# Kernel optimization log

Hardware: AMD Instinct MI355X
Metric: run time of the kernel (lower is better)

## Reference

```python
import jax, jax.numpy as jnp
import numpy as np

# Quantum kernel closed form:
#   Encoder applies RY(x_k) on wire k from |0>, then RY(-y_k); RY(-y)RY(x) = RY(x-y).
#   Amplitude of |0...0> = prod_k <0|RY(x_k - y_k)|0> = prod_k cos((x_k - y_k)/2).
#   kernel(x, y) = | prod_k cos((x_k - y_k)/2) |.
# Using cos(a-b) = cos a cos b + sin a sin b avoids forming explicit pairwise diffs twice.

def setup_inputs() -> dict:
    key = jax.random.key(0)
    x = jax.random.normal(key, (32, 1024, 4), dtype=jnp.float32)  # [B, S, n_wires]
    return {"x": x}


def reference(x) -> jnp.ndarray:
    c = jnp.cos(0.5 * x)  # [B, S, W]
    s = jnp.sin(0.5 * x)
    # cos((x_i,k - x_j,k)/2) for all pairs -> [B, S, S, W]
    term = c[:, :, None, :] * c[:, None, :, :] + s[:, :, None, :] * s[:, None, :, :]
    kernel_mat = jnp.abs(jnp.prod(term, axis=-1))  # [B, S, S]
    attn = jax.nn.softmax(kernel_mat, axis=-1)
    return jnp.matmul(attn, x)  # [B, S, W]
```

## Files before the change

kernel.cpp:

```cpp
#include <hip/hip_runtime.h>


typedef _Float16 f16x8 __attribute__((ext_vector_type(8)));
typedef _Float16 h2    __attribute__((ext_vector_type(2)));
typedef float    f32x16 __attribute__((ext_vector_type(16)));
typedef unsigned int u32x4 __attribute__((ext_vector_type(4)));

#define SQ 1024
#define NTHREADS 512
#define ROWS 64

#if __has_builtin(__builtin_amdgcn_permlane32_swap)
__device__ __forceinline__ void pl32swap(unsigned &a, unsigned &b) {
    auto r = __builtin_amdgcn_permlane32_swap(a, b, false, false);
    a = r[0]; b = r[1];
}
#else
__device__ __forceinline__ void pl32swap(unsigned &a, unsigned &b) {
    asm("v_permlane32_swap_b32 %0, %1" : "+v"(a), "+v"(b));
}
#endif

__device__ __forceinline__ unsigned pexp_abs(float a, float b) {
    auto tp = __builtin_amdgcn_cvt_pkrtz(fabsf(a), fabsf(b));
    h2 t = __builtin_bit_cast(h2, tp);
    const h2 C4 = {(_Float16)0.0695580f, (_Float16)0.0695580f};
    const h2 C3 = {(_Float16)0.1399810f, (_Float16)0.1399810f};
    const h2 C2 = {(_Float16)0.5100530f, (_Float16)0.5100530f};
    const h2 C1 = {(_Float16)0.9986730f, (_Float16)0.9986730f};
    const h2 C0 = {(_Float16)0.9999940f, (_Float16)0.9999940f};
    h2 p = __builtin_elementwise_fma(C4, t, C3);
    p = __builtin_elementwise_fma(p, t, C2);
    p = __builtin_elementwise_fma(p, t, C1);
    p = __builtin_elementwise_fma(p, t, C0);
    return __builtin_bit_cast(unsigned, p);
}

__global__ __launch_bounds__(NTHREADS, 4)
void qka_kernel(const float* __restrict__ x, float* __restrict__ out) {
    __shared__ f16x8 lds_F0[SQ];
    __shared__ f16x8 lds_F1[SQ];
    __shared__ f16x8 lds_XT[5 * 129];

    const int bid   = blockIdx.x;
    const int b     = bid >> 4;
    const int Ibase = (bid & 15) * ROWS;
    const int tid   = threadIdx.x;

    const float4* xb  = (const float4*)(x + (size_t)b * SQ * 4);
    _Float16*     xtp = (_Float16*)lds_XT;

    #pragma unroll
    for (int k = 0; k < SQ / NTHREADS; ++k) {
        int j = tid + k * NTHREADS;
        float4 v = xb[j];
        float c0 = __cosf(0.5f * v.x), s0 = __sinf(0.5f * v.x);
        float c1 = __cosf(0.5f * v.y), s1 = __sinf(0.5f * v.y);
        float c2 = __cosf(0.5f * v.z), s2 = __sinf(0.5f * v.z);
        float c3 = __cosf(0.5f * v.w), s3 = __sinf(0.5f * v.w);
        float m0 = c0 * c1, m1 = s0 * c1, m2 = c0 * s1, m3 = s0 * s1;
        float n0 = m0 * c2, n1 = m1 * c2, n2 = m2 * c2, n3 = m3 * c2;
        float n4 = m0 * s2, n5 = m1 * s2, n6 = m2 * s2, n7 = m3 * s2;
        f16x8 p0, p1;
        p0[0] = (_Float16)(n0 * c3); p0[1] = (_Float16)(n1 * c3);
        p0[2] = (_Float16)(n2 * c3); p0[3] = (_Float16)(n3 * c3);
        p0[4] = (_Float16)(n4 * c3); p0[5] = (_Float16)(n5 * c3);
        p0[6] = (_Float16)(n6 * c3); p0[7] = (_Float16)(n7 * c3);
        p1[0] = (_Float16)(n0 * s3); p1[1] = (_Float16)(n1 * s3);
        p1[2] = (_Float16)(n2 * s3); p1[3] = (_Float16)(n3 * s3);
        p1[4] = (_Float16)(n4 * s3); p1[5] = (_Float16)(n5 * s3);
        p1[6] = (_Float16)(n6 * s3); p1[7] = (_Float16)(n7 * s3);
        int sj = j ^ ((j >> 3) & 7);
        lds_F0[sj] = p0;
        lds_F1[sj] = p1;
        xtp[0 * 1032 + j] = (_Float16)v.x;
        xtp[1 * 1032 + j] = (_Float16)v.y;
        xtp[2 * 1032 + j] = (_Float16)v.z;
        xtp[3 * 1032 + j] = (_Float16)v.w;
        xtp[4 * 1032 + j] = (_Float16)1.0f;
    }
    __syncthreads();

    const int wid  = tid >> 6;
    const int q    = wid & 3;
    const int rt   = wid >> 2;
    const int lane = tid & 63;
    const int h    = lane >> 5;
    const int ln   = lane & 31;

    const f16x8* Fh = h ? lds_F1 : lds_F0;
    int ib = Ibase + rt * 32 + ln; ib ^= (ib >> 3) & 7;
    const f16x8 bfrag = Fh[ib];

    const int rowsel = (ln < 4) ? ln : 4;
    const int xbase  = rowsel * 129 + q * 32 + h;

    f32x16 oacc0 = (f32x16)(0.0f);
    f32x16 oacc1 = (f32x16)(0.0f);

    int ja0 = q * 256 + ln;
    f16x8 af0 = Fh[ja0 ^ ((ja0 >> 3) & 7)];
    f32x16 d = __builtin_amdgcn_mfma_f32_32x32x16_f16(
        af0, bfrag, (f32x16)(0.0f), 0, 0, 0);

    #pragma unroll 2
    for (int t = 0; t < 8; ++t) {
        f16x8 afn;
        if (t < 7) {
            int jn = q * 256 + (t + 1) * 32 + ln;
            afn = Fh[jn ^ ((jn >> 3) & 7)];
        }
        f16x8 xf0 = lds_XT[xbase + t * 4];
        f16x8 xf1 = lds_XT[xbase + t * 4 + 2];
        unsigned q0 = pexp_abs(d[0],  d[1]);
        unsigned q1 = pexp_abs(d[2],  d[3]);
        unsigned q2 = pexp_abs(d[4],  d[5]);
        unsigned q3 = pexp_abs(d[6],  d[7]);
        unsigned q4 = pexp_abs(d[8],  d[9]);
        unsigned q5 = pexp_abs(d[10], d[11]);
        unsigned q6 = pexp_abs(d[12], d[13]);
        unsigned q7 = pexp_abs(d[14], d[15]);
        f32x16 dn;
        if (t < 7)
            dn = __builtin_amdgcn_mfma_f32_32x32x16_f16(
                afn, bfrag, (f32x16)(0.0f), 0, 0, 0);
        pl32swap(q0, q2); pl32swap(q1, q3);
        pl32swap(q4, q6); pl32swap(q5, q7);
        u32x4 w0 = {q0, q1, q2, q3};
        u32x4 w1 = {q4, q5, q6, q7};
        f16x8 ef0 = __builtin_bit_cast(f16x8, w0);
        f16x8 ef1 = __builtin_bit_cast(f16x8, w1);
        oacc0 = __builtin_amdgcn_mfma_f32_32x32x16_f16(ef0, xf0, oacc0, 0, 0, 0);
        oacc1 = __builtin_amdgcn_mfma_f32_32x32x16_f16(ef1, xf1, oacc1, 0, 0, 0);
        if (t < 7) d = dn;
    }

    __syncthreads();
    float* ps = (float*)lds_F0;
    if (ln < 5) {
        #pragma unroll
        for (int r = 0; r < 16; ++r) {
            int m = (r & 3) + 8 * (r >> 2) + 4 * h;
            ps[(q * 64 + rt * 32 + m) * 8 + ln] = oacc0[r] + oacc1[r];
        }
    }
    __syncthreads();

    if (tid < ROWS) {
        float nx = 0.f, ny = 0.f, nz = 0.f, nw = 0.f, den = 0.f;
        #pragma unroll
        for (int qq = 0; qq < 4; ++qq) {
            const float* p = &ps[(qq * 64 + tid) * 8];
            nx += p[0]; ny += p[1]; nz += p[2]; nw += p[3]; den += p[4];
        }
        float inv = 1.0f / den;
        ((float4*)out)[(size_t)b * SQ + Ibase + tid] =
            make_float4(nx * inv, ny * inv, nz * inv, nw * inv);
    }
}

extern "C" void kernel_launch(void* const* d_in, const int* in_sizes, int n_in,
                              void* d_out, int out_size, void* d_ws, size_t ws_size,
                              hipStream_t stream) {
    const float* x = (const float*)d_in[0];
    float* out = (float*)d_out;
    dim3 grid(32 * (SQ / ROWS));
    dim3 block(NTHREADS);
    qka_kernel<<<grid, block, 0, stream>>>(x, out);
}
```

Baseline: 12.13 us.

## Precompute feature maps in a staging kernel and DMA them into LDS

Moves the per-token cos/sin feature-map computation and the x transpose into a separate staging kernel that writes fp16 features to workspace, once per batch instead of once per each of 16 row blocks. The main kernel then fills LDS with direct global-to-LDS loads, applying the swizzle on the global address side. This removes redundant transcendental work across blocks but adds a second launch and a round trip of the features through global memory.

Measured after the change: 17.70 us. 45.9% more time.

```diff
diff --git a/kernel.cpp b/kernel.cpp
--- a/kernel.cpp
+++ b/kernel.cpp
@@ -9,6 +9,13 @@
 #define SQ 1024
 #define NTHREADS 512
 #define ROWS 64
+#define XT_SLOTS 645
+#define XT_PITCH 1032
+
+#define F0_OFF 0
+#define F1_OFF (32 * 1024 * 16)
+#define XT_OFF (2 * 32 * 1024 * 16)
+#define XT_BATCH_BYTES (704 * 16)
 
 #if __has_builtin(__builtin_amdgcn_permlane32_swap)
 __device__ __forceinline__ void pl32swap(unsigned &a, unsigned &b) {
@@ -36,49 +43,73 @@
     return __builtin_bit_cast(unsigned, p);
 }
 
+__global__ __launch_bounds__(512)
+void qka_stage(const float* __restrict__ x, char* __restrict__ ws) {
+    const int bid = blockIdx.x;
+    const int b   = bid >> 1;
+    const int j   = ((bid & 1) << 9) + threadIdx.x;
+    float4 v = ((const float4*)(x + (size_t)b * SQ * 4))[j];
+    float c0 = __cosf(0.5f * v.x), s0 = __sinf(0.5f * v.x);
+    float c1 = __cosf(0.5f * v.y), s1 = __sinf(0.5f * v.y);
+    float c2 = __cosf(0.5f * v.z), s2 = __sinf(0.5f * v.z);
+    float c3 = __cosf(0.5f * v.w), s3 = __sinf(0.5f * v.w);
+    float m0 = c0 * c1, m1 = s0 * c1, m2 = c0 * s1, m3 = s0 * s1;
+    float n0 = m0 * c2, n1 = m1 * c2, n2 = m2 * c2, n3 = m3 * c2;
+    float n4 = m0 * s2, n5 = m1 * s2, n6 = m2 * s2, n7 = m3 * s2;
+    f16x8 p0, p1;
+    p0[0] = (_Float16)(n0 * c3); p0[1] = (_Float16)(n1 * c3);
+    p0[2] = (_Float16)(n2 * c3); p0[3] = (_Float16)(n3 * c3);
+    p0[4] = (_Float16)(n4 * c3); p0[5] = (_Float16)(n5 * c3);
+    p0[6] = (_Float16)(n6 * c3); p0[7] = (_Float16)(n7 * c3);
+    p1[0] = (_Float16)(n0 * s3); p1[1] = (_Float16)(n1 * s3);
+    p1[2] = (_Float16)(n2 * s3); p1[3] = (_Float16)(n3 * s3);
+    p1[4] = (_Float16)(n4 * s3); p1[5] = (_Float16)(n5 * s3);
+    p1[6] = (_Float16)(n6 * s3); p1[7] = (_Float16)(n7 * s3);
+    ((f16x8*)(ws + F0_OFF))[b * SQ + j] = p0;
+    ((f16x8*)(ws + F1_OFF))[b * SQ + j] = p1;
+    _Float16* xt = (_Float16*)(ws + XT_OFF + (size_t)b * XT_BATCH_BYTES);
+    xt[0 * XT_PITCH + j] = (_Float16)v.x;
+    xt[1 * XT_PITCH + j] = (_Float16)v.y;
+    xt[2 * XT_PITCH + j] = (_Float16)v.z;
+    xt[3 * XT_PITCH + j] = (_Float16)v.w;
+    xt[4 * XT_PITCH + j] = (_Float16)1.0f;
+}
+
 __global__ __launch_bounds__(NTHREADS, 4)
-void qka_kernel(const float* __restrict__ x, float* __restrict__ out) {
+void qka_kernel(const char* __restrict__ ws, float* __restrict__ out) {
     __shared__ f16x8 lds_F0[SQ];
     __shared__ f16x8 lds_F1[SQ];
-    __shared__ f16x8 lds_XT[5 * 129];
+    __shared__ f16x8 lds_XT[XT_SLOTS];
 
     const int bid   = blockIdx.x;
     const int b     = bid >> 4;
     const int Ibase = (bid & 15) * ROWS;
     const int tid   = threadIdx.x;
 
-    const float4* xb  = (const float4*)(x + (size_t)b * SQ * 4);
-    _Float16*     xtp = (_Float16*)lds_XT;
-
-    #pragma unroll
-    for (int k = 0; k < SQ / NTHREADS; ++k) {
-        int j = tid + k * NTHREADS;
-        float4 v = xb[j];
-        float c0 = __cosf(0.5f * v.x), s0 = __sinf(0.5f * v.x);
-        float c1 = __cosf(0.5f * v.y), s1 = __sinf(0.5f * v.y);
-        float c2 = __cosf(0.5f * v.z), s2 = __sinf(0.5f * v.z);
-        float c3 = __cosf(0.5f * v.w), s3 = __sinf(0.5f * v.w);
-        float m0 = c0 * c1, m1 = s0 * c1, m2 = c0 * s1, m3 = s0 * s1;
-        float n0 = m0 * c2, n1 = m1 * c2, n2 = m2 * c2, n3 = m3 * c2;
-        float n4 = m0 * s2, n5 = m1 * s2, n6 = m2 * s2, n7 = m3 * s2;
-        f16x8 p0, p1;
-        p0[0] = (_Float16)(n0 * c3); p0[1] = (_Float16)(n1 * c3);
-        p0[2] = (_Float16)(n2 * c3); p0[3] = (_Float16)(n3 * c3);
-        p0[4] = (_Float16)(n4 * c3); p0[5] = (_Float16)(n5 * c3);
-        p0[6] = (_Float16)(n6 * c3); p0[7] = (_Float16)(n7 * c3);
-        p1[0] = (_Float16)(n0 * s3); p1[1] = (_Float16)(n1 * s3);
-        p1[2] = (_Float16)(n2 * s3); p1[3] = (_Float16)(n3 * s3);
-        p1[4] = (_Float16)(n4 * s3); p1[5] = (_Float16)(n5 * s3);
-        p1[6] = (_Float16)(n6 * s3); p1[7] = (_Float16)(n7 * s3);
-        int sj = j ^ ((j >> 3) & 7);
-        lds_F0[sj] = p0;
-        lds_F1[sj] = p1;
-        xtp[0 * 1032 + j] = (_Float16)v.x;
-        xtp[1 * 1032 + j] = (_Float16)v.y;
-        xtp[2 * 1032 + j] = (_Float16)v.z;
-        xtp[3 * 1032 + j] = (_Float16)v.w;
-        xtp[4 * 1032 + j] = (_Float16)1.0f;
-    }
+    const f16x8* F0g = (const f16x8*)(ws + F0_OFF) + (size_t)b * SQ;
+    const f16x8* F1g = (const f16x8*)(ws + F1_OFF) + (size_t)b * SQ;
+    const f16x8* XTg = (const f16x8*)(ws + XT_OFF + (size_t)b * XT_BATCH_BYTES);
+
+    {
+        const int w    = tid >> 6;
+        const int ln64 = tid & 63;
+        #pragma unroll
+        for (int i = 0; i < 2; ++i) {
+            int base = w * 128 + i * 64;
+            int l    = base + ln64;
+            int s    = l ^ ((l >> 3) & 7);
+            __builtin_amdgcn_global_load_lds(
+                (const __attribute__((address_space(1))) unsigned int*)&F0g[s],
+                (__attribute__((address_space(3))) unsigned int*)&lds_F0[base],
+                16, 0, 0);
+            __builtin_amdgcn_global_load_lds(
+                (const __attribute__((address_space(1))) unsigned int*)&F1g[s],
+                (__attribute__((address_space(3))) unsigned int*)&lds_F1[base],
+                16, 0, 0);
+        }
+    }
+    for (int t = tid; t < XT_SLOTS; t += NTHREADS)
+        lds_XT[t] = XTg[t];
     __syncthreads();
 
     const int wid  = tid >> 6;
@@ -164,7 +195,7 @@
                               hipStream_t stream) {
     const float* x = (const float*)d_in[0];
     float* out = (float*)d_out;
-    dim3 grid(32 * (SQ / ROWS));
-    dim3 block(NTHREADS);
-    qka_kernel<<<grid, block, 0, stream>>>(x, out);
-}
+    char* ws = (char*)d_ws;
+    qka_stage<<<dim3(64), dim3(512), 0, stream>>>(x, ws);
+    qka_kernel<<<dim3(32 * (SQ / ROWS)), dim3(NTHREADS), 0, stream>>>(ws, out);
+}
```

## Halve block size and make each wave build its own LDS feature slice

Applied to the files above, without the earlier changes.

Blocks shrink from 512 to 256 threads and handle 32 query rows instead of 64, so the grid doubles. Each wave now computes the trig features and the transposed-x values only for the 256-key slice it consumes. That removes the block-wide barrier between the setup phase and the MFMA loop. The query-side B fragment is built directly in registers rather than read back from LDS. The cost is that the per-key feature computation is repeated across twice as many blocks.

Measured after the change: 14.05 us. 1.16x slower.

```diff
diff --git a/kernel.cpp b/kernel.cpp
--- a/kernel.cpp
+++ b/kernel.cpp
@@ -7,8 +7,8 @@
 typedef unsigned int u32x4 __attribute__((ext_vector_type(4)));
 
 #define SQ 1024
-#define NTHREADS 512
-#define ROWS 64
+#define NTHREADS 256
+#define ROWS 32
 
 #if __has_builtin(__builtin_amdgcn_permlane32_swap)
 __device__ __forceinline__ void pl32swap(unsigned &a, unsigned &b) {
@@ -36,6 +36,24 @@
     return __builtin_bit_cast(unsigned, p);
 }
 
+__device__ __forceinline__ void fhalves(float4 v, f16x8 &p0, f16x8 &p1) {
+    float c0 = __cosf(0.5f * v.x), s0 = __sinf(0.5f * v.x);
+    float c1 = __cosf(0.5f * v.y), s1 = __sinf(0.5f * v.y);
+    float c2 = __cosf(0.5f * v.z), s2 = __sinf(0.5f * v.z);
+    float c3 = __cosf(0.5f * v.w), s3 = __sinf(0.5f * v.w);
+    float m0 = c0 * c1, m1 = s0 * c1, m2 = c0 * s1, m3 = s0 * s1;
+    float n0 = m0 * c2, n1 = m1 * c2, n2 = m2 * c2, n3 = m3 * c2;
+    float n4 = m0 * s2, n5 = m1 * s2, n6 = m2 * s2, n7 = m3 * s2;
+    p0[0] = (_Float16)(n0 * c3); p0[1] = (_Float16)(n1 * c3);
+    p0[2] = (_Float16)(n2 * c3); p0[3] = (_Float16)(n3 * c3);
+    p0[4] = (_Float16)(n4 * c3); p0[5] = (_Float16)(n5 * c3);
+    p0[6] = (_Float16)(n6 * c3); p0[7] = (_Float16)(n7 * c3);
+    p1[0] = (_Float16)(n0 * s3); p1[1] = (_Float16)(n1 * s3);
+    p1[2] = (_Float16)(n2 * s3); p1[3] = (_Float16)(n3 * s3);
+    p1[4] = (_Float16)(n4 * s3); p1[5] = (_Float16)(n5 * s3);
+    p1[6] = (_Float16)(n6 * s3); p1[7] = (_Float16)(n7 * s3);
+}
+
 __global__ __launch_bounds__(NTHREADS, 4)
 void qka_kernel(const float* __restrict__ x, float* __restrict__ out) {
     __shared__ f16x8 lds_F0[SQ];
@@ -43,62 +61,67 @@
     __shared__ f16x8 lds_XT[5 * 129];
 
     const int bid   = blockIdx.x;
-    const int b     = bid >> 4;
-    const int Ibase = (bid & 15) * ROWS;
+    const int b     = bid >> 5;
+    const int Ibase = (bid & 31) * ROWS;
     const int tid   = threadIdx.x;
+
+    const int q    = tid >> 6;
+    const int lane = tid & 63;
+    const int h    = lane >> 5;
+    const int ln   = lane & 31;
 
     const float4* xb  = (const float4*)(x + (size_t)b * SQ * 4);
     _Float16*     xtp = (_Float16*)lds_XT;
 
-    #pragma unroll
-    for (int k = 0; k < SQ / NTHREADS; ++k) {
-        int j = tid + k * NTHREADS;
-        float4 v = xb[j];
-        float c0 = __cosf(0.5f * v.x), s0 = __sinf(0.5f * v.x);
-        float c1 = __cosf(0.5f * v.y), s1 = __sinf(0.5f * v.y);
-        float c2 = __cosf(0.5f * v.z), s2 = __sinf(0.5f * v.z);
-        float c3 = __cosf(0.5f * v.w), s3 = __sinf(0.5f * v.w);
+    const int jbase = q * 256;
+    float4 vI = xb[Ibase + ln];
+    float4 v0 = xb[jbase + lane];
+    float4 v1 = xb[jbase + lane + 64];
+    float4 v2 = xb[jbase + lane + 128];
+    float4 v3 = xb[jbase + lane + 192];
+
+    f16x8 bfrag;
+    {
+        float c0 = __cosf(0.5f * vI.x), s0 = __sinf(0.5f * vI.x);
+        float c1 = __cosf(0.5f * vI.y), s1 = __sinf(0.5f * vI.y);
+        float c2 = __cosf(0.5f * vI.z), s2 = __sinf(0.5f * vI.z);
+        float c3 = __cosf(0.5f * vI.w), s3 = __sinf(0.5f * vI.w);
+        float w3 = h ? s3 : c3;
         float m0 = c0 * c1, m1 = s0 * c1, m2 = c0 * s1, m3 = s0 * s1;
         float n0 = m0 * c2, n1 = m1 * c2, n2 = m2 * c2, n3 = m3 * c2;
         float n4 = m0 * s2, n5 = m1 * s2, n6 = m2 * s2, n7 = m3 * s2;
-        f16x8 p0, p1;
-        p0[0] = (_Float16)(n0 * c3); p0[1] = (_Float16)(n1 * c3);
-        p0[2] = (_Float16)(n2 * c3); p0[3] = (_Float16)(n3 * c3);
-        p0[4] = (_Float16)(n4 * c3); p0[5] = (_Float16)(n5 * c3);
-        p0[6] = (_Float16)(n6 * c3); p0[7] = (_Float16)(n7 * c3);
-        p1[0] = (_Float16)(n0 * s3); p1[1] = (_Float16)(n1 * s3);
-        p1[2] = (_Float16)(n2 * s3); p1[3] = (_Float16)(n3 * s3);
-        p1[4] = (_Float16)(n4 * s3); p1[5] = (_Float16)(n5 * s3);
-        p1[6] = (_Float16)(n6 * s3); p1[7] = (_Float16)(n7 * s3);
-        int sj = j ^ ((j >> 3) & 7);
-        lds_F0[sj] = p0;
-        lds_F1[sj] = p1;
-        xtp[0 * 1032 + j] = (_Float16)v.x;
-        xtp[1 * 1032 + j] = (_Float16)v.y;
-        xtp[2 * 1032 + j] = (_Float16)v.z;
-        xtp[3 * 1032 + j] = (_Float16)v.w;
-        xtp[4 * 1032 + j] = (_Float16)1.0f;
+        bfrag[0] = (_Float16)(n0 * w3); bfrag[1] = (_Float16)(n1 * w3);
+        bfrag[2] = (_Float16)(n2 * w3); bfrag[3] = (_Float16)(n3 * w3);
+        bfrag[4] = (_Float16)(n4 * w3); bfrag[5] = (_Float16)(n5 * w3);
+        bfrag[6] = (_Float16)(n6 * w3); bfrag[7] = (_Float16)(n7 * w3);
     }
-    __syncthreads();
 
-    const int wid  = tid >> 6;
-    const int q    = wid & 3;
-    const int rt   = wid >> 2;
-    const int lane = tid & 63;
-    const int h    = lane >> 5;
-    const int ln   = lane & 31;
+    {
+        float4 vv[4] = {v0, v1, v2, v3};
+        #pragma unroll
+        for (int i = 0; i < 4; ++i) {
+            int j = jbase + lane + i * 64;
+            f16x8 p0, p1;
+            fhalves(vv[i], p0, p1);
+            int sj = j ^ ((j >> 3) & 7);
+            lds_F0[sj] = p0;
+            lds_F1[sj] = p1;
+            xtp[0 * 1032 + j] = (_Float16)vv[i].x;
+            xtp[1 * 1032 + j] = (_Float16)vv[i].y;
+            xtp[2 * 1032 + j] = (_Float16)vv[i].z;
+            xtp[3 * 1032 + j] = (_Float16)vv[i].w;
+            xtp[4 * 1032 + j] = (_Float16)1.0f;
+        }
+    }
 
     const f16x8* Fh = h ? lds_F1 : lds_F0;
-    int ib = Ibase + rt * 32 + ln; ib ^= (ib >> 3) & 7;
-    const f16x8 bfrag = Fh[ib];
-
     const int rowsel = (ln < 4) ? ln : 4;
     const int xbase  = rowsel * 129 + q * 32 + h;
 
     f32x16 oacc0 = (f32x16)(0.0f);
     f32x16 oacc1 = (f32x16)(0.0f);
 
-    int ja0 = q * 256 + ln;
+    int ja0 = jbase + ln;
     f16x8 af0 = Fh[ja0 ^ ((ja0 >> 3) & 7)];
     f32x16 d = __builtin_amdgcn_mfma_f32_32x32x16_f16(
         af0, bfrag, (f32x16)(0.0f), 0, 0, 0);
@@ -107,7 +130,7 @@
     for (int t = 0; t < 8; ++t) {
         f16x8 afn;
         if (t < 7) {
-            int jn = q * 256 + (t + 1) * 32 + ln;
+            int jn = jbase + (t + 1) * 32 + ln;
             afn = Fh[jn ^ ((jn >> 3) & 7)];
         }
         f16x8 xf0 = lds_XT[xbase + t * 4];
@@ -141,7 +164,7 @@
         #pragma unroll
         for (int r = 0; r < 16; ++r) {
             int m = (r & 3) + 8 * (r >> 2) + 4 * h;
-            ps[(q * 64 + rt * 32 + m) * 8 + ln] = oacc0[r] + oacc1[r];
+            ps[(q * 32 + m) * 8 + ln] = oacc0[r] + oacc1[r];
         }
     }
     __syncthreads();
@@ -150,7 +173,7 @@
         float nx = 0.f, ny = 0.f, nz = 0.f, nw = 0.f, den = 0.f;
         #pragma unroll
         for (int qq = 0; qq < 4; ++qq) {
-            const float* p = &ps[(qq * 64 + tid) * 8];
+            const float* p = &ps[(qq * 32 + tid) * 8];
             nx += p[0]; ny += p[1]; nz += p[2]; nw += p[3]; den += p[4];
         }
         float inv = 1.0f / den;
```
